# Performance work log

Hardware: AMD Instinct MI355X
Metric: run time of the kernel (lower is better)

Reference implementation:

```python
import jax, jax.numpy as jnp
import numpy as np

N = 524288
IN_C = 128
OUT_C = 128
NUM_GRAPHS = 64
NUM_STROKES = 8192
EPS = 1e-5


def setup_inputs() -> dict:
    key = jax.random.key(0)
    ks = jax.random.split(key, 8)
    x = jax.random.normal(ks[0], (N, IN_C), dtype=jnp.float32)
    batch = jnp.sort(jax.random.randint(ks[1], (N,), 0, NUM_GRAPHS))
    stroke_idx = jnp.sort(jax.random.randint(ks[2], (N,), 0, NUM_STROKES))
    s = 1.0 / np.sqrt(IN_C)
    W_max = jax.random.uniform(ks[3], (IN_C, OUT_C), jnp.float32, -s, s)
    b_max = jax.random.uniform(ks[4], (OUT_C,), jnp.float32, -s, s)
    g_max = jnp.ones((OUT_C,), jnp.float32)
    be_max = jnp.zeros((OUT_C,), jnp.float32)
    W_sk = jax.random.uniform(ks[5], (IN_C, OUT_C), jnp.float32, -s, s)
    b_sk = jax.random.uniform(ks[6], (OUT_C,), jnp.float32, -s, s)
    g_sk = jnp.ones((OUT_C,), jnp.float32)
    be_sk = jnp.zeros((OUT_C,), jnp.float32)
    return {"x": x, "batch": batch, "stroke_idx": stroke_idx,
            "W_max": W_max, "b_max": b_max, "g_max": g_max, "be_max": be_max,
            "W_sk": W_sk, "b_sk": b_sk, "g_sk": g_sk, "be_sk": be_sk}


def _mlp(x, W, b, gamma, beta):
    # Linear -> BatchNorm1d (training-mode batch stats, biased var) -> ReLU
    h = x @ W + b
    mu = jnp.mean(h, axis=0)
    var = jnp.mean((h - mu) ** 2, axis=0)
    h = (h - mu) * jax.lax.rsqrt(var + EPS) * gamma + beta
    return jax.nn.relu(h)


def reference(x, batch, stroke_idx, W_max, b_max, g_max, be_max, W_sk, b_sk, g_sk, be_sk):
    pool_max = _mlp(x, W_max, b_max, g_max, be_max)      # (N, F)
    pool_sketch = _mlp(x, W_sk, b_sk, g_sk, be_sk)       # (N, F)
    # segment max-pool per graph / per stroke, then broadcast back to nodes
    gmax = jax.ops.segment_max(pool_max, batch, num_segments=NUM_GRAPHS)       # (G, F)
    smax = jax.ops.segment_max(pool_sketch, stroke_idx, num_segments=NUM_STROKES)  # (S, F)
    pool_max = gmax[batch]          # (N, F)
    pool_sketch = smax[stroke_idx]  # (N, F)
    return jnp.concatenate([pool_sketch, pool_max], axis=1)  # (N, 2F)
```

## Files before the change

### kernel.cpp

```cpp
#include <hip/hip_runtime.h>
#include <hip/hip_bf16.h>
#include <climits>
#include <cstdint>
#include <cfloat>

#define NROWS   524288
#define KDIM    128
#define NGRAPH  64
#define NSTROKE 8192
#define EPSF    1e-5f

typedef __bf16 bf16x8 __attribute__((ext_vector_type(8)));
typedef float  f32x4  __attribute__((ext_vector_type(4)));

#define WT_OFF    0
#define CSUM_OFF  65536
#define CSQ_OFF   66560
#define ST_OFF    67584
#define GT_OFF    (ST_OFF + NSTROKE*KDIM*4)

__device__ __forceinline__ unsigned short f2bf(float f) {
  unsigned int u = __float_as_uint(f);
  u += 0x7fffu + ((u >> 16) & 1u);
  return (unsigned short)(u >> 16);
}
__device__ __forceinline__ int fkey(float f) {
  int b = __float_as_int(f);
  return b >= 0 ? b : (b ^ 0x7fffffff);
}
__device__ __forceinline__ float fdec(int k) {
  int b = k >= 0 ? k : (k ^ 0x7fffffff);
  return __int_as_float(b);
}

__global__ void k_init(const float* __restrict__ Wmax, const float* __restrict__ Wsk,
                       unsigned char* __restrict__ ws) {
  unsigned short* wt = (unsigned short*)(ws + WT_OFF);
  float* csum = (float*)(ws + CSUM_OFF);
  float* csq  = (float*)(ws + CSQ_OFF);
  int* st = (int*)(ws + ST_OFF);
  int* gt = (int*)(ws + GT_OFF);
  int i = blockIdx.x * blockDim.x + threadIdx.x;
  const int total = NSTROKE * KDIM;
  for (; i < total; i += gridDim.x * blockDim.x) {
    st[i] = INT_MIN;
    if (i < NGRAPH * KDIM) gt[i] = INT_MIN;
    if (i < 256) { csum[i] = 0.f; csq[i] = 0.f; }
    if (i < 256 * KDIM) {
      int c = i / KDIM, k = i % KDIM;
      float w = (c < 128) ? Wsk[k * 128 + c] : Wmax[k * 128 + (c - 128)];
      wt[i] = f2bf(w);
    }
  }
}

__global__ __launch_bounds__(512, 4) void k_pass1(const float* __restrict__ x,
                                                  const int* __restrict__ batch,
                                                  const int* __restrict__ stroke,
                                                  unsigned char* __restrict__ ws) {
  __shared__ __align__(16) unsigned short xs[2][64 * 128];
  const unsigned short* wt = (const unsigned short*)(ws + WT_OFF);
  float* csum = (float*)(ws + CSUM_OFF);
  float* csq  = (float*)(ws + CSQ_OFF);
  int* st = (int*)(ws + ST_OFF);
  int* gt = (int*)(ws + GT_OFF);

  const int tid  = threadIdx.x;
  const int lane = tid & 63;
  const int wv   = tid >> 6;
  const int lr   = lane & 15;
  const int lg   = lane >> 4;
  const int srow = tid >> 3;
  const int skg  = tid & 7;

  const int colbase = wv * 32;
  const bool isS = (wv < 4);
  const int* __restrict__ segp = isS ? stroke : batch;
  int* __restrict__ tab = isS ? st : gt;
  const int tcol = colbase - (isS ? 0 : 128);

  bf16x8 bfrag[4][2];
#pragma unroll
  for (int ks = 0; ks < 4; ++ks)
#pragma unroll
    for (int n = 0; n < 2; ++n)
      bfrag[ks][n] = *(const bf16x8*)(wt + (colbase + n * 16 + lr) * KDIM + ks * 32 + lg * 8);

  float sumn[2] = {0.f, 0.f};
  float sqn[2]  = {0.f, 0.f};

  int   curseg = -1;
  float runmax[2] = {-FLT_MAX, -FLT_MAX};

#define FLUSH()                                                               \
  if (curseg >= 0) {                                                          \
    _Pragma("unroll")                                                         \
    for (int n = 0; n < 2; ++n) {                                             \
      float f = runmax[n];                                                    \
      f = fmaxf(f, __shfl_xor(f, 16));                                        \
      f = fmaxf(f, __shfl_xor(f, 32));                                        \
      if (lg == 0) atomicMax(&tab[curseg * KDIM + tcol + n * 16 + lr], fkey(f)); \
    }                                                                         \
  }

#define PF_LOAD(ROW0)                                                         \
  {                                                                           \
    const float* src = x + (size_t)((ROW0) + srow) * KDIM + skg * 16;         \
    pf[0] = *(const f32x4*)src;                                               \
    pf[1] = *(const f32x4*)(src + 4);                                         \
    pf[2] = *(const f32x4*)(src + 8);                                         \
    pf[3] = *(const f32x4*)(src + 12);                                        \
  }

#define PF_STORE(P)                                                           \
  {                                                                           \
    union { bf16x8 v; unsigned short u[8]; } pk;                              \
    pk.u[0] = f2bf(pf[0][0]); pk.u[1] = f2bf(pf[0][1]);                       \
    pk.u[2] = f2bf(pf[0][2]); pk.u[3] = f2bf(pf[0][3]);                       \
    pk.u[4] = f2bf(pf[1][0]); pk.u[5] = f2bf(pf[1][1]);                       \
    pk.u[6] = f2bf(pf[1][2]); pk.u[7] = f2bf(pf[1][3]);                       \
    *(bf16x8*)(xs[P] + srow * KDIM + (((skg * 2) ^ (srow & 7)) << 3)) = pk.v; \
    pk.u[0] = f2bf(pf[2][0]); pk.u[1] = f2bf(pf[2][1]);                       \
    pk.u[2] = f2bf(pf[2][2]); pk.u[3] = f2bf(pf[2][3]);                       \
    pk.u[4] = f2bf(pf[3][0]); pk.u[5] = f2bf(pf[3][1]);                       \
    pk.u[6] = f2bf(pf[3][2]); pk.u[7] = f2bf(pf[3][3]);                       \
    *(bf16x8*)(xs[P] + srow * KDIM + (((skg * 2 + 1) ^ (srow & 7)) << 3)) = pk.v; \
  }

  const int brow = blockIdx.x * 512;
  f32x4 pf[4];
  int segv, segnext;

  PF_LOAD(brow);
  segv = segp[brow + lane];
  PF_STORE(0);
  __syncthreads();

  int cur = 0;
  for (int ti = 0; ti < 8; ++ti) {
    if (ti < 7) {
      PF_LOAD(brow + (ti + 1) * 64);
      segnext = segp[brow + (ti + 1) * 64 + lane];
    }

    f32x4 acc[4][2];
#pragma unroll
    for (int m = 0; m < 4; ++m)
#pragma unroll
      for (int n = 0; n < 2; ++n) { f32x4 z = {0.f, 0.f, 0.f, 0.f}; acc[m][n] = z; }

#pragma unroll
    for (int ks = 0; ks < 4; ++ks) {
      bf16x8 af[4];
#pragma unroll
      for (int m = 0; m < 4; ++m) {
        int r  = m * 16 + lr;
        int kg = ks * 4 + lg;
        af[m] = *(const bf16x8*)(xs[cur] + r * KDIM + ((kg ^ (r & 7)) << 3));
      }
#pragma unroll
      for (int m = 0; m < 4; ++m) {
        acc[m][0] = __builtin_amdgcn_mfma_f32_16x16x32_bf16(af[m], bfrag[ks][0], acc[m][0], 0, 0, 0);
        acc[m][1] = __builtin_amdgcn_mfma_f32_16x16x32_bf16(af[m], bfrag[ks][1], acc[m][1], 0, 0, 0);
      }
    }

    float tm[2];
#pragma unroll
    for (int n = 0; n < 2; ++n) {
      float s = 0.f, q = 0.f, t = -FLT_MAX;
#pragma unroll
      for (int m = 0; m < 4; ++m)
#pragma unroll
        for (int rg = 0; rg < 4; ++rg) {
          float v = acc[m][n][rg];
          s += v; q = fmaf(v, v, q); t = fmaxf(t, v);
        }
      sumn[n] += s; sqn[n] += q; tm[n] = t;
    }

    {
      int pv = __shfl_up(segv, 1);
      unsigned long long mask = __ballot(lane > 0 && pv != segv);
      if (mask == 0ull) {
        int seg0 = __shfl(segv, 0);
        if (seg0 == curseg) {
#pragma unroll
          for (int n = 0; n < 2; ++n) runmax[n] = fmaxf(runmax[n], tm[n]);
        } else {
          FLUSH();
          curseg = seg0;
#pragma unroll
          for (int n = 0; n < 2; ++n) runmax[n] = tm[n];
        }
      } else {
        unsigned long long rem = mask;
        int a = 0;
        while (true) {
          int b = rem ? (int)__builtin_ctzll(rem) : 64;
          int segr = __shfl(segv, a);
          float rm[2] = {-FLT_MAX, -FLT_MAX};
#pragma unroll
          for (int m = 0; m < 4; ++m)
#pragma unroll
            for (int rg = 0; rg < 4; ++rg) {
              int pos = m * 16 + lg * 4 + rg;
              bool in = (pos >= a) && (pos < b);
#pragma unroll
              for (int n = 0; n < 2; ++n)
                rm[n] = in ? fmaxf(rm[n], acc[m][n][rg]) : rm[n];
            }
          if (a == 0 && segr == curseg) {
#pragma unroll
            for (int n = 0; n < 2; ++n) runmax[n] = fmaxf(runmax[n], rm[n]);
          } else {
            FLUSH();
            curseg = segr;
#pragma unroll
            for (int n = 0; n < 2; ++n) runmax[n] = rm[n];
          }
          if (b >= 64) break;
          rem &= rem - 1; a = b;
        }
      }
    }

    if (ti < 7) {
      PF_STORE(cur ^ 1);
      segv = segnext;
    }
    __syncthreads();
    cur ^= 1;
  }

  FLUSH();

#pragma unroll
  for (int n = 0; n < 2; ++n) {
    float s = sumn[n], q = sqn[n];
    s += __shfl_xor(s, 16); s += __shfl_xor(s, 32);
    q += __shfl_xor(q, 16); q += __shfl_xor(q, 32);
    if (lg == 0) {
      atomicAdd(&csum[colbase + n * 16 + lr], s);
      atomicAdd(&csq [colbase + n * 16 + lr], q);
    }
  }
#undef FLUSH
#undef PF_LOAD
#undef PF_STORE
}

__global__ __launch_bounds__(256) void k_out(const int* __restrict__ batch,
                                             const int* __restrict__ stroke,
                                             const float* __restrict__ g_max,
                                             const float* __restrict__ be_max,
                                             const float* __restrict__ g_sk,
                                             const float* __restrict__ be_sk,
                                             const unsigned char* __restrict__ ws,
                                             float* __restrict__ out) {
  const float* csum = (const float*)(ws + CSUM_OFF);
  const float* csq  = (const float*)(ws + CSQ_OFF);
  const int* st = (const int*)(ws + ST_OFF);
  const int* gt = (const int*)(ws + GT_OFF);

  const int lane = threadIdx.x & 63;
  const int wvid = blockIdx.x * 4 + (threadIdx.x >> 6);
  const int row0 = wvid * 64;
  const bool isS = lane < 32;
  const int  cg  = (isS ? lane : lane - 32) * 4;
  const int* tab  = isS ? st : gt;
  const int* idxp = isS ? stroke : batch;
  const float* gv = isS ? g_sk : g_max;
  const float* bv = isS ? be_sk : be_max;

  const float invN = 1.0f / (float)NROWS;
  f32x4 mu, sc, bb;
#pragma unroll
  for (int j = 0; j < 4; ++j) {
    int cc = (isS ? 0 : 128) + cg + j;
    float m  = csum[cc] * invN;
    float vr = csq[cc] * invN - m * m;
    mu[j] = m;
    sc[j] = gv[cg + j] * rsqrtf(vr + EPSF);
    bb[j] = bv[cg + j];
  }

  f32x4* out4 = (f32x4*)out;
#pragma unroll 4
  for (int r = 0; r < 64; ++r) {
    int row = row0 + r;
    int seg = idxp[row];
    const int4 k4 = *(const int4*)(tab + (size_t)seg * KDIM + cg);
    f32x4 v;
    v[0] = fdec(k4.x); v[1] = fdec(k4.y); v[2] = fdec(k4.z); v[3] = fdec(k4.w);
#pragma unroll
    for (int j = 0; j < 4; ++j) v[j] = fmaxf(0.f, (v[j] - mu[j]) * sc[j] + bb[j]);
    __builtin_nontemporal_store(v, &out4[(size_t)row * 64 + lane]);
  }
}

extern "C" void kernel_launch(void* const* d_in, const int* in_sizes, int n_in,
                              void* d_out, int out_size, void* d_ws, size_t ws_size,
                              hipStream_t stream) {
  const float* x      = (const float*)d_in[0];
  const int*   batch  = (const int*)d_in[1];
  const int*   stroke = (const int*)d_in[2];
  const float* Wmax   = (const float*)d_in[3];
  const float* g_max  = (const float*)d_in[5];
  const float* be_max = (const float*)d_in[6];
  const float* Wsk    = (const float*)d_in[7];
  const float* g_sk   = (const float*)d_in[9];
  const float* be_sk  = (const float*)d_in[10];
  unsigned char* ws = (unsigned char*)d_ws;
  float* out = (float*)d_out;

  k_init <<<2048, 512, 0, stream>>>(Wmax, Wsk, ws);
  k_pass1<<<1024, 512, 0, stream>>>(x, batch, stroke, ws);
  k_out  <<<2048, 256, 0, stream>>>(batch, stroke, g_max, be_max, g_sk, be_sk, ws, out);
}
```

Measured before the change: 235.4 us.

## Pre-convert x to swizzled bf16 and stream tiles via global_load_lds

Adds a separate kernel that converts x from fp32 to bf16 with the LDS swizzle pre-applied in a workspace buffer. The main GEMM/segment-max kernel then copies tiles directly global-to-LDS with global_load_lds, dropping register staging and in-loop conversion. This frees registers and simplifies the pipeline, but adds an extra full pass over x: read fp32, write bf16, reread bf16. It also relaxes the occupancy hint on launch bounds.

```diff
diff --git a/kernel.cpp b/kernel.cpp
--- a/kernel.cpp
+++ b/kernel.cpp
@@ -17,7 +17,8 @@
 #define CSUM_OFF  65536
 #define CSQ_OFF   66560
 #define ST_OFF    67584
-#define GT_OFF    (ST_OFF + NSTROKE*KDIM*4)
+#define GT_OFF    (ST_OFF + (size_t)NSTROKE*KDIM*4)
+#define XB_OFF    (GT_OFF + (size_t)NGRAPH*KDIM*4)
 
 __device__ __forceinline__ unsigned short f2bf(float f) {
   unsigned int u = __float_as_uint(f);
@@ -31,6 +32,18 @@
 __device__ __forceinline__ float fdec(int k) {
   int b = k >= 0 ? k : (k ^ 0x7fffffff);
   return __int_as_float(b);
+}
+__device__ __forceinline__ bf16x8 cvt8(f32x4 a, f32x4 b) {
+  bf16x8 r;
+  r[0] = (__bf16)a[0]; r[1] = (__bf16)a[1]; r[2] = (__bf16)a[2]; r[3] = (__bf16)a[3];
+  r[4] = (__bf16)b[0]; r[5] = (__bf16)b[1]; r[6] = (__bf16)b[2]; r[7] = (__bf16)b[3];
+  return r;
+}
+
+typedef const __attribute__((address_space(1))) void* as1p;
+typedef __attribute__((address_space(3))) void* as3p;
+__device__ __forceinline__ void gload_lds16(const void* g, void* l) {
+  __builtin_amdgcn_global_load_lds((as1p)g, (as3p)l, 16, 0, 0);
 }
 
 __global__ void k_init(const float* __restrict__ Wmax, const float* __restrict__ Wsk,
@@ -54,12 +67,28 @@
   }
 }
 
-__global__ __launch_bounds__(512, 4) void k_pass1(const float* __restrict__ x,
-                                                  const int* __restrict__ batch,
-                                                  const int* __restrict__ stroke,
-                                                  unsigned char* __restrict__ ws) {
+__global__ __launch_bounds__(256) void k_conv(const float* __restrict__ x,
+                                              unsigned char* __restrict__ ws) {
+  unsigned short* xb = (unsigned short*)(ws + XB_OFF);
+  int i = blockIdx.x * blockDim.x + threadIdx.x;
+  const int total = NROWS * (KDIM / 8);
+  for (; i < total; i += gridDim.x * blockDim.x) {
+    int row = i >> 4;
+    int kg  = i & 15;
+    const f32x4* src = (const f32x4*)(x + (size_t)row * KDIM + kg * 8);
+    f32x4 a = __builtin_nontemporal_load(src);
+    f32x4 b = __builtin_nontemporal_load(src + 1);
+    int kgd = kg ^ (row & 7);
+    *(bf16x8*)(xb + (size_t)row * KDIM + kgd * 8) = cvt8(a, b);
+  }
+}
+
+__global__ __launch_bounds__(512) void k_pass1(const int* __restrict__ batch,
+                                               const int* __restrict__ stroke,
+                                               unsigned char* __restrict__ ws) {
   __shared__ __align__(16) unsigned short xs[2][64 * 128];
   const unsigned short* wt = (const unsigned short*)(ws + WT_OFF);
+  const unsigned short* xb = (const unsigned short*)(ws + XB_OFF);
   float* csum = (float*)(ws + CSUM_OFF);
   float* csq  = (float*)(ws + CSQ_OFF);
   int* st = (int*)(ws + ST_OFF);
@@ -70,8 +99,6 @@
   const int wv   = tid >> 6;
   const int lr   = lane & 15;
   const int lg   = lane >> 4;
-  const int srow = tid >> 3;
-  const int skg  = tid & 7;
 
   const int colbase = wv * 32;
   const bool isS = (wv < 4);
@@ -88,7 +115,6 @@
 
   float sumn[2] = {0.f, 0.f};
   float sqn[2]  = {0.f, 0.f};
-
   int   curseg = -1;
   float runmax[2] = {-FLT_MAX, -FLT_MAX};
 
@@ -103,43 +129,25 @@
     }                                                                         \
   }
 
-#define PF_LOAD(ROW0)                                                         \
+#define STAGE(T, B)                                                           \
   {                                                                           \
-    const float* src = x + (size_t)((ROW0) + srow) * KDIM + skg * 16;         \
-    pf[0] = *(const f32x4*)src;                                               \
-    pf[1] = *(const f32x4*)(src + 4);                                         \
-    pf[2] = *(const f32x4*)(src + 8);                                         \
-    pf[3] = *(const f32x4*)(src + 12);                                        \
-  }
-
-#define PF_STORE(P)                                                           \
-  {                                                                           \
-    union { bf16x8 v; unsigned short u[8]; } pk;                              \
-    pk.u[0] = f2bf(pf[0][0]); pk.u[1] = f2bf(pf[0][1]);                       \
-    pk.u[2] = f2bf(pf[0][2]); pk.u[3] = f2bf(pf[0][3]);                       \
-    pk.u[4] = f2bf(pf[1][0]); pk.u[5] = f2bf(pf[1][1]);                       \
-    pk.u[6] = f2bf(pf[1][2]); pk.u[7] = f2bf(pf[1][3]);                       \
-    *(bf16x8*)(xs[P] + srow * KDIM + (((skg * 2) ^ (srow & 7)) << 3)) = pk.v; \
-    pk.u[0] = f2bf(pf[2][0]); pk.u[1] = f2bf(pf[2][1]);                       \
-    pk.u[2] = f2bf(pf[2][2]); pk.u[3] = f2bf(pf[2][3]);                       \
-    pk.u[4] = f2bf(pf[3][0]); pk.u[5] = f2bf(pf[3][1]);                       \
-    pk.u[6] = f2bf(pf[3][2]); pk.u[7] = f2bf(pf[3][3]);                       \
-    *(bf16x8*)(xs[P] + srow * KDIM + (((skg * 2 + 1) ^ (srow & 7)) << 3)) = pk.v; \
+    const char* gb = (const char*)(xb + (size_t)(brow + (T) * 64 + wv * 8) * KDIM) + lane * 16; \
+    char* lb = (char*)(&xs[B][(wv * 8) * KDIM]);                              \
+    gload_lds16(gb, lb);                                                      \
+    gload_lds16(gb + 1024, lb + 1024);                                        \
   }
 
   const int brow = blockIdx.x * 512;
-  f32x4 pf[4];
-  int segv, segnext;
-
-  PF_LOAD(brow);
+  int segv, segnext = 0;
+
+  STAGE(0, 0);
   segv = segp[brow + lane];
-  PF_STORE(0);
   __syncthreads();
 
   int cur = 0;
   for (int ti = 0; ti < 8; ++ti) {
     if (ti < 7) {
-      PF_LOAD(brow + (ti + 1) * 64);
+      STAGE(ti + 1, cur ^ 1);
       segnext = segp[brow + (ti + 1) * 64 + lane];
     }
 
@@ -225,11 +233,8 @@
       }
     }
 
-    if (ti < 7) {
-      PF_STORE(cur ^ 1);
-      segv = segnext;
-    }
     __syncthreads();
+    if (ti < 7) segv = segnext;
     cur ^= 1;
   }
 
@@ -246,8 +251,7 @@
     }
   }
 #undef FLUSH
-#undef PF_LOAD
-#undef PF_STORE
+#undef STAGE
 }
 
 __global__ __launch_bounds__(256) void k_out(const int* __restrict__ batch,
@@ -315,6 +319,7 @@
   float* out = (float*)d_out;
 
   k_init <<<2048, 512, 0, stream>>>(Wmax, Wsk, ws);
-  k_pass1<<<1024, 512, 0, stream>>>(x, batch, stroke, ws);
+  k_conv <<<2048, 256, 0, stream>>>(x, ws);
+  k_pass1<<<1024, 512, 0, stream>>>(batch, stroke, ws);
   k_out  <<<2048, 256, 0, stream>>>(batch, stroke, g_max, be_max, g_sk, be_sk, ws, out);
 }
```

Measured after the change: 266.0 us. +13.0%, slower.
